# Optimization experiments

Hardware: AMD Instinct MI355X
Metric: run time of the kernel (lower is better)

The kernel has to match this reference:

```python
import jax, jax.numpy as jnp
import numpy as np

B, S, D = 2, 2048, 1024
H, DH = 16, 64
DM = 4096
NEG = 1e10


def setup_inputs() -> dict:
    key = jax.random.key(0)
    ks = jax.random.split(key, 8)
    sc = 1.0 / np.sqrt(D)
    return {
        "x": jax.random.normal(ks[0], (B, S, D), jnp.float32),
        "W_Q": jax.random.normal(ks[1], (H, DH, D), jnp.float32) * sc,
        "W_K": jax.random.normal(ks[2], (H, DH, D), jnp.float32) * sc,
        "W_V": jax.random.normal(ks[3], (H, DH, D), jnp.float32) * sc,
        "W_O": jax.random.normal(ks[4], (D, H * DH), jnp.float32) * sc,
        "W_in": jax.random.normal(ks[5], (DM, D), jnp.float32) * sc,
        "b_in": jnp.zeros((DM,), jnp.float32),
        "W_out": jax.random.normal(ks[6], (D, DM), jnp.float32) * sc,
        "b_out": jnp.zeros((D,), jnp.float32),
    }


def reference(x, W_Q, W_K, W_V, W_O, W_in, b_in, W_out, b_out):
    b, s, d = x.shape
    d_head = W_Q.shape[1]
    # --- Attention (faithful to original einsum/mask formulation) ---
    q = jnp.einsum('ihd,bpd->biph', W_Q, x)
    k = jnp.einsum('ihd,bpd->biph', W_K, x)
    v = jnp.einsum('ihd,bpd->biph', W_V, x)
    scores = jnp.einsum('biph,biqh->biqp', k, q)  # [b,i,q,p]
    # original: t.tril(scores) - 1e10 * (1 - triu(ones)) ; mask buffer is triu
    triu = jnp.triu(jnp.ones((s, s), x.dtype))
    masked = jnp.tril(scores) - NEG * (1.0 - triu)
    attn = jax.nn.softmax(masked / np.sqrt(d_head), axis=-1)
    z = jnp.einsum('biph,biqp->biqh', v, attn)          # [b,i,q,h]
    z_flat = z.transpose(0, 2, 1, 3).reshape(b, s, -1)   # b q (i h)
    attn_out = jnp.einsum('df,bqf->bqd', W_O, z_flat)
    # --- Block residual structure (as written: x = attn(x); x = x + x) ---
    mid = attn_out + attn_out
    # --- MLP ---
    pre = jnp.einsum('md,bpd->bpm', W_in, mid) + b_in
    h = jax.nn.relu(pre)
    mlp_out = jnp.einsum('dm,bpm->bpd', W_out, h) + b_out
    return mid + mlp_out
```

## Files before the change

kernel.cpp:

```cpp
#include <hip/hip_runtime.h>
#include <hip/hip_bf16.h>
#include <stdint.h>

typedef unsigned short ushort_t;
typedef __attribute__((ext_vector_type(8))) short short8;
typedef __attribute__((ext_vector_type(4))) float floatx4;

#define DEV __device__ __forceinline__

DEV ushort_t f2b(float f) {
  uint32_t x = __float_as_uint(f);
  uint32_t r = (x + 0x7FFFu + ((x >> 16) & 1u)) >> 16;
  return (ushort_t)r;
}
DEV float b2f(ushort_t u) { return __uint_as_float(((uint32_t)u) << 16); }

DEV void async16(const ushort_t* g, ushort_t* l) {
  __builtin_amdgcn_global_load_lds(
      (const __attribute__((address_space(1))) void*)g,
      (__attribute__((address_space(3))) void*)l, 16, 0, 0);
}

struct Cvt7 {
  const float* src[7];
  ushort_t* dst[7];
  float scale[7];
  unsigned start[8];
};
__global__ void cvt_all(Cvt7 a) {
  unsigned idx = blockIdx.x * blockDim.x + threadIdx.x;
  if (idx >= a.start[7]) return;
  int seg = 0;
#pragma unroll
  for (int j = 1; j < 7; j++) seg += (idx >= a.start[j]) ? 1 : 0;
  unsigned off = idx - a.start[seg];
  float sc = a.scale[seg];
  float4 v = ((const float4*)a.src[seg])[off];
  ((ushort4*)a.dst[seg])[off] =
      make_ushort4(f2b(v.x * sc), f2b(v.y * sc), f2b(v.z * sc), f2b(v.w * sc));
}

template <int MODE, int MT, int SWZ>
__launch_bounds__(256)
__global__ void gemm_bt(const ushort_t* __restrict__ A, const ushort_t* __restrict__ Bm,
                        int M, int N, int Kd, int ldk,
                        ushort_t* __restrict__ outB, float* __restrict__ outF,
                        const float* __restrict__ bias) {
  constexpr int TM = 32 * MT;
  __shared__ alignas(16) ushort_t As[TM * 64];
  __shared__ alignas(16) ushort_t Bs[128 * 64];
  const int tid = threadIdx.x;
  const int wave = tid >> 6, lane = tid & 63;
  const int wm = wave >> 1, wn = wave & 1;

  int bx, by;
  if constexpr (SWZ == 1) {
    const int f = blockIdx.x + gridDim.x * blockIdx.y;
    by = (f & 7) + 8 * (f / (8 * gridDim.x));
    bx = (f >> 3) % gridDim.x;
  } else if constexpr (SWZ == 2) {
    const int x = blockIdx.x, y = blockIdx.y;
    bx = 2 * (x & 3) + (y & 1);
    by = (y >> 1) + 32 * (x >> 2);
  } else {
    bx = blockIdx.x; by = blockIdx.y;
  }
  const int m0 = by * TM, n0 = bx * 128;
  const int kz = blockIdx.z * Kd;

  floatx4 acc[MT][4];
#pragma unroll
  for (int i = 0; i < MT; i++)
#pragma unroll
    for (int j = 0; j < 4; j++) acc[i][j] = (floatx4){0.f, 0.f, 0.f, 0.f};

  const int r8 = lane >> 3;
  const int scol = (((lane & 7) ^ (r8 & 7)) * 8);
  const ushort_t* gA = A + (size_t)(m0 + wave * (TM / 4) + r8) * ldk + kz + scol;
  const ushort_t* gB = Bm + (size_t)(n0 + wave * 32 + r8) * ldk + kz + scol;
  ushort_t* lA = As + wave * (TM / 4) * 64;
  ushort_t* lB = Bs + wave * 2048;

  const int fr = lane & 15, fq = lane >> 4;
  const int sw = fr & 7;
  const ushort_t* rdA = As + (wm * 16 * MT + fr) * 64;
  const ushort_t* rdB = Bs + (wn * 64 + fr) * 64;

  for (int k0 = 0; k0 < Kd; k0 += 64) {
#pragma unroll
    for (int j = 0; j < MT; j++) async16(gA + (size_t)j * 8 * ldk, lA + j * 512);
#pragma unroll
    for (int j = 0; j < 4; j++) async16(gB + (size_t)j * 8 * ldk, lB + j * 512);
    gA += 64; gB += 64;
    __syncthreads();
#pragma unroll
    for (int h = 0; h < 2; h++) {
      const int co = ((h * 4 + fq) ^ sw) * 8;
      short8 af[MT], bfv[4];
#pragma unroll
      for (int mt = 0; mt < MT; mt++) af[mt] = *(const short8*)(rdA + mt * 16 * 64 + co);
#pragma unroll
      for (int nt = 0; nt < 4; nt++) bfv[nt] = *(const short8*)(rdB + nt * 16 * 64 + co);
#pragma unroll
      for (int mt = 0; mt < MT; mt++)
#pragma unroll
        for (int nt = 0; nt < 4; nt++)
          acc[mt][nt] = __builtin_amdgcn_mfma_f32_16x16x32_bf16(af[mt], bfv[nt], acc[mt][nt], 0, 0, 0);
    }
    __syncthreads();
  }

  const int crow = m0 + wm * 16 * MT + (lane >> 4) * 4;
  const int ccol = n0 + wn * 64 + (lane & 15);
#pragma unroll
  for (int mt = 0; mt < MT; mt++)
#pragma unroll
    for (int nt = 0; nt < 4; nt++) {
      floatx4 a = acc[mt][nt];
#pragma unroll
      for (int r = 0; r < 4; r++) {
        const int gm = crow + mt * 16 + r;
        const int gn = ccol + nt * 16;
        const size_t idx = (size_t)gm * N + gn;
        float v = a[r];
        if constexpr (MODE == 0) {
          outB[idx] = f2b(v);
        } else if constexpr (MODE == 1) {
          outB[idx] = f2b(v);
          outF[idx] = v + bias[gn];
        } else if constexpr (MODE == 2) {
          float t = v + bias[gn];
          outB[idx] = f2b(t > 0.f ? t : 0.f);
        } else if constexpr (MODE == 5) {
          unsafeAtomicAdd(&outF[idx], v);
        }
      }
    }
}

template <int MODE>
__launch_bounds__(512, 2)
__global__ void gemm256(const ushort_t* __restrict__ A, const ushort_t* __restrict__ Bm,
                        int M, int N, int Kd, int ldk,
                        ushort_t* __restrict__ outB, float* __restrict__ outF,
                        const float* __restrict__ bias) {
  __shared__ alignas(16) ushort_t As[4][256 * 32];
  __shared__ alignas(16) ushort_t Bs[4][256 * 32];
  const int tid = threadIdx.x;
  const int lane = tid & 63;
  const int wave = tid >> 6;
  const int wm = wave >> 2, wn = wave & 3;

  const int gy = gridDim.y;
  int f = blockIdx.x + gridDim.x * blockIdx.y;
  {
    const int nwg = gridDim.x * gy;
    const int q = nwg >> 3, rr = nwg & 7;
    const int xcd = f & 7, ix = f >> 3;
    f = (xcd < rr ? xcd * (q + 1) : rr * (q + 1) + (xcd - rr) * q) + ix;
  }
  const int bx = f / gy, by = f - gy * bx;
  const int m0 = by * 256, n0 = bx * 256;
  const size_t kz = (size_t)blockIdx.z * Kd;

  floatx4 acc[8][4];
#pragma unroll
  for (int i = 0; i < 8; i++)
#pragma unroll
    for (int j = 0; j < 4; j++) acc[i][j] = (floatx4){0.f, 0.f, 0.f, 0.f};

  const int rloc = tid >> 2, cch = tid & 3;
  const int gcol = ((cch ^ ((rloc >> 1) & 3)) * 8);
  const ushort_t* gA = A + (size_t)(m0 + rloc) * ldk + kz + gcol;
  const ushort_t* gB = Bm + (size_t)(n0 + rloc) * ldk + kz + gcol;
  const int lofs = rloc * 32 + cch * 8;

#define STGA32(bufi, kofs)                                              \
  {                                                                     \
    async16(gA + (kofs), &As[bufi][lofs]);                              \
    async16(gA + (size_t)128 * ldk + (kofs), &As[bufi][4096 + lofs]);   \
  }
#define STGB32(bufi, kofs)                                              \
  {                                                                     \
    async16(gB + (kofs), &Bs[bufi][lofs]);                              \
    async16(gB + (size_t)128 * ldk + (kofs), &Bs[bufi][4096 + lofs]);   \
  }

  const int NT = Kd >> 5;
  STGA32(0, 0) STGB32(0, 0)
  if (NT > 1) { STGA32(1, 32) STGB32(1, 32) }
  if (NT > 2) { STGA32(2, 64) STGB32(2, 64) }
  if (NT > 2) asm volatile("s_waitcnt vmcnt(8)" ::: "memory");
  else if (NT > 1) asm volatile("s_waitcnt vmcnt(4)" ::: "memory");
  else asm volatile("s_waitcnt vmcnt(0)" ::: "memory");
  __builtin_amdgcn_s_barrier();

  const int fr = lane & 15, fq = lane >> 4;
  const int co = ((fq ^ ((fr >> 1) & 3)) * 8);
  const int aoff = (wm * 128 + fr) * 32 + co;
  const int boff = (wn * 64 + fr) * 32 + co;

  for (int kt = 0; kt < NT; ++kt) {
    const int cb = kt & 3;
    const int pb = (kt + 3) & 3;
    const int kof = (kt + 3) * 32;
    const bool sp = (kt + 3) < NT;
    const ushort_t* Ab = As[cb];
    const ushort_t* Bb = Bs[cb];
    short8 av[4], bv[4];

#pragma unroll
    for (int i = 0; i < 4; i++) av[i] = *(const short8*)(Ab + aoff + i * 512);
#pragma unroll
    for (int j = 0; j < 4; j++) bv[j] = *(const short8*)(Bb + boff + j * 512);
    if (sp) STGA32(pb, kof)
    __builtin_amdgcn_s_barrier();
    asm volatile("s_waitcnt lgkmcnt(0)" ::: "memory");
    __builtin_amdgcn_s_setprio(1);
#pragma unroll
    for (int i = 0; i < 4; i++)
#pragma unroll
      for (int j = 0; j < 4; j++)
        acc[i][j] = __builtin_amdgcn_mfma_f32_16x16x32_bf16(av[i], bv[j], acc[i][j], 0, 0, 0);
    __builtin_amdgcn_s_setprio(0);
    __builtin_amdgcn_s_barrier();

#pragma unroll
    for (int i = 0; i < 4; i++) av[i] = *(const short8*)(Ab + aoff + 2048 + i * 512);
    if (sp) STGB32(pb, kof)
    __builtin_amdgcn_s_barrier();
    asm volatile("s_waitcnt lgkmcnt(0)" ::: "memory");
    __builtin_amdgcn_s_setprio(1);
#pragma unroll
    for (int i = 0; i < 4; i++)
#pragma unroll
      for (int j = 0; j < 4; j++)
        acc[4 + i][j] = __builtin_amdgcn_mfma_f32_16x16x32_bf16(av[i], bv[j], acc[4 + i][j], 0, 0, 0);
    __builtin_amdgcn_s_setprio(0);
    if (kt + 3 < NT) asm volatile("s_waitcnt vmcnt(8)" ::: "memory");
    else if (kt + 2 < NT) asm volatile("s_waitcnt vmcnt(4)" ::: "memory");
    else asm volatile("s_waitcnt vmcnt(0)" ::: "memory");
    __builtin_amdgcn_s_barrier();
  }
#undef STGA32
#undef STGB32

  const int crow = m0 + wm * 128 + (lane >> 4) * 4;
  const int ccol = n0 + wn * 64 + (lane & 15);
#pragma unroll
  for (int mt = 0; mt < 8; mt++)
#pragma unroll
    for (int nt = 0; nt < 4; nt++) {
      floatx4 a = acc[mt][nt];
#pragma unroll
      for (int r = 0; r < 4; r++) {
        const int gm = crow + mt * 16 + r;
        const int gn = ccol + nt * 16;
        const size_t idx = (size_t)gm * N + gn;
        if constexpr (MODE == 0) {
          outB[idx] = f2b(a[r]);
        } else if constexpr (MODE == 2) {
          float t = a[r] + bias[gn];
          outB[idx] = f2b(t > 0.f ? t : 0.f);
        } else {
          outF[idx] = a[r];
        }
      }
    }
}

__launch_bounds__(256)
__global__ void attn1(const ushort_t* __restrict__ qkv,
                      float* __restrict__ eG, float* __restrict__ psumG) {
  const int c = blockIdx.x & 63;
  const int i = (blockIdx.x >> 6) & 15;
  const int b = blockIdx.x >> 10;
  const int t = threadIdx.x, wave = t >> 6, h = t & 63;
  const size_t rowbase = (size_t)b * 2048 * 3072;
  float vacc = 0.f;
#pragma unroll
  for (int r = 0; r < 8; r++) {
    const int s = c * 32 + wave * 8 + r;
    const size_t rb = rowbase + (size_t)s * 3072 + i * 64 + h;
    float q = b2f(qkv[rb]);
    float k = b2f(qkv[rb + 1024]);
    float v = b2f(qkv[rb + 2048]);
    float d = q * k;
#pragma unroll
    for (int off = 32; off > 0; off >>= 1) d += __shfl_xor(d, off, 64);
    if (h == 0) eG[((size_t)(b * 16 + i)) * 2048 + s] = __expf(d * 0.125f);
    vacc += v;
  }
  __shared__ float vs[4][64];
  vs[wave][h] = vacc;
  __syncthreads();
  if (t < 64)
    psumG[(((size_t)(b * 16 + i)) * 64 + c) * 64 + t] =
        vs[0][t] + vs[1][t] + vs[2][t] + vs[3][t];
}

__launch_bounds__(256)
__global__ void attn2(const ushort_t* __restrict__ qkv,
                      const float* __restrict__ eG, const float* __restrict__ psumG,
                      ushort_t* __restrict__ Z) {
  const int wave = threadIdx.x >> 6, h = threadIdx.x & 63;
  const int c = (blockIdx.x & 15) * 4 + wave;
  const int i = (blockIdx.x >> 4) & 15;
  const int b = blockIdx.x >> 8;
  const size_t rowbase = (size_t)b * 2048 * 3072;
  const size_t pbase = ((size_t)(b * 16 + i)) * 64;
  float run = 0.f;
#pragma unroll 8
  for (int cc = c + 1; cc < 64; cc++) run += psumG[(pbase + cc) * 64 + h];
  const size_t ebase = ((size_t)(b * 16 + i)) * 2048;
  for (int t4 = 1; t4 >= 0; t4--) {
    float vv[16], ee[16];
#pragma unroll
    for (int j = 0; j < 16; j++) {
      const int s = c * 32 + t4 * 16 + j;
      vv[j] = b2f(qkv[rowbase + (size_t)s * 3072 + 2048 + i * 64 + h]);
      ee[j] = eG[ebase + s];
    }
#pragma unroll
    for (int j = 15; j >= 0; j--) {
      const int s = c * 32 + t4 * 16 + j;
      float z = (ee[j] * vv[j] + run) / (ee[j] + (float)(2047 - s));
      Z[((size_t)b * 2048 + s) * 1024 + i * 64 + h] = f2b(z);
      run += vv[j];
    }
  }
}

extern "C" void kernel_launch(void* const* d_in, const int* in_sizes, int n_in,
                              void* d_out, int out_size, void* d_ws, size_t ws_size,
                              hipStream_t stream) {
  const float* x     = (const float*)d_in[0];
  const float* W_Q   = (const float*)d_in[1];
  const float* W_K   = (const float*)d_in[2];
  const float* W_V   = (const float*)d_in[3];
  const float* W_O   = (const float*)d_in[4];
  const float* W_in  = (const float*)d_in[5];
  const float* b_in  = (const float*)d_in[6];
  const float* W_out = (const float*)d_in[7];
  const float* b_out = (const float*)d_in[8];
  float* out = (float*)d_out;

  char* base = (char*)d_ws;
  const size_t MB = 1048576;
  ushort_t* Xb    = (ushort_t*)(base + 0 * MB);
  ushort_t* Wqkv  = (ushort_t*)(base + 8 * MB);
  ushort_t* WOb   = (ushort_t*)(base + 14 * MB);
  ushort_t* Z     = (ushort_t*)(base + 16 * MB);
  ushort_t* QKV   = (ushort_t*)(base + 24 * MB);
  ushort_t* midb  = (ushort_t*)(base + 48 * MB);
  ushort_t* Winb  = (ushort_t*)(base + 56 * MB);
  ushort_t* Woutb = (ushort_t*)(base + 64 * MB);
  ushort_t* Hb    = (ushort_t*)(base + 72 * MB);
  float*    psumG = (float*)(base + 72 * MB);
  float*    eG    = (float*)(base + 72 * MB + 524288);

  Cvt7 ca;
  ca.src[0] = x;     ca.dst[0] = Xb;               ca.scale[0] = 1.f;
  ca.src[1] = W_Q;   ca.dst[1] = Wqkv;             ca.scale[1] = 1.f;
  ca.src[2] = W_K;   ca.dst[2] = Wqkv + 1048576;   ca.scale[2] = 1.f;
  ca.src[3] = W_V;   ca.dst[3] = Wqkv + 2097152;   ca.scale[3] = 1.f;
  ca.src[4] = W_O;   ca.dst[4] = WOb;              ca.scale[4] = 2.f;
  ca.src[5] = W_in;  ca.dst[5] = Winb;             ca.scale[5] = 1.f;
  ca.src[6] = W_out; ca.dst[6] = Woutb;            ca.scale[6] = 1.f;
  unsigned n4s[7] = {1048576, 262144, 262144, 262144, 262144, 1048576, 1048576};
  unsigned acc4 = 0;
  for (int j = 0; j < 7; j++) { ca.start[j] = acc4; acc4 += n4s[j]; }
  ca.start[7] = acc4;
  cvt_all<<<dim3((acc4 + 255) / 256), dim3(256), 0, stream>>>(ca);

  gemm_bt<0, 4, 0><<<dim3(24, 32), 256, 0, stream>>>(Xb, Wqkv, 4096, 3072, 1024, 1024,
                                                     QKV, nullptr, nullptr);
  attn1<<<dim3(2048), 256, 0, stream>>>(QKV, eG, psumG);
  attn2<<<dim3(512), 256, 0, stream>>>(QKV, eG, psumG, Z);
  gemm_bt<1, 2, 1><<<dim3(8, 64), 256, 0, stream>>>(Z, WOb, 4096, 1024, 1024, 1024,
                                                    midb, out, b_out);
  gemm256<2><<<dim3(16, 16), 512, 0, stream>>>(midb, Winb, 4096, 4096, 1024, 1024,
                                               Hb, nullptr, b_in);
  gemm_bt<5, 2, 2><<<dim3(8, 64, 2), 256, 0, stream>>>(Hb, Woutb, 4096, 1024, 2048, 4096,
                                                       nullptr, out, nullptr);
}
```

Baseline: 286.5 us.

## Rewrite 256x256 GEMM with BK=64 double buffering and use it for QKV projection

Replaces the 4-stage BK=32 pipeline of the 256x256 GEMM with a 2-stage BK=64 double buffer using a new swizzled LDS layout. The MFMA work is split into four quadrant phases so A and B fragments are reused across phases with fewer LDS reads. The QKV projection also moves from the smaller-tile gemm_bt kernel to this 256-tile kernel, launched on a 12x16 grid. Risks: prefetch depth is only one stage and waits on vmcnt(0) every iteration, and the QKV grid of 192 blocks may underfill the GPU.

```diff
diff --git a/kernel.cpp b/kernel.cpp
--- a/kernel.cpp
+++ b/kernel.cpp
@@ -140,12 +140,12 @@
 
 template <int MODE>
 __launch_bounds__(512, 2)
-__global__ void gemm256(const ushort_t* __restrict__ A, const ushort_t* __restrict__ Bm,
-                        int M, int N, int Kd, int ldk,
-                        ushort_t* __restrict__ outB, float* __restrict__ outF,
-                        const float* __restrict__ bias) {
-  __shared__ alignas(16) ushort_t As[4][256 * 32];
-  __shared__ alignas(16) ushort_t Bs[4][256 * 32];
+__global__ void gemm256v2(const ushort_t* __restrict__ A, const ushort_t* __restrict__ Bm,
+                          int M, int N, int Kd, int ldk,
+                          ushort_t* __restrict__ outB, float* __restrict__ outF,
+                          const float* __restrict__ bias) {
+  __shared__ alignas(16) ushort_t As[2][2][8192];
+  __shared__ alignas(16) ushort_t Bs[2][2][8192];
   const int tid = threadIdx.x;
   const int lane = tid & 63;
   const int wave = tid >> 6;
@@ -169,81 +169,116 @@
 #pragma unroll
     for (int j = 0; j < 4; j++) acc[i][j] = (floatx4){0.f, 0.f, 0.f, 0.f};
 
-  const int rloc = tid >> 2, cch = tid & 3;
-  const int gcol = ((cch ^ ((rloc >> 1) & 3)) * 8);
-  const ushort_t* gA = A + (size_t)(m0 + rloc) * ldk + kz + gcol;
-  const ushort_t* gB = Bm + (size_t)(n0 + rloc) * ldk + kz + gcol;
-  const int lofs = rloc * 32 + cch * 8;
-
-#define STGA32(bufi, kofs)                                              \
-  {                                                                     \
-    async16(gA + (kofs), &As[bufi][lofs]);                              \
-    async16(gA + (size_t)128 * ldk + (kofs), &As[bufi][4096 + lofs]);   \
-  }
-#define STGB32(bufi, kofs)                                              \
-  {                                                                     \
-    async16(gB + (kofs), &Bs[bufi][lofs]);                              \
-    async16(gB + (size_t)128 * ldk + (kofs), &Bs[bufi][4096 + lofs]);   \
-  }
-
-  const int NT = Kd >> 5;
-  STGA32(0, 0) STGB32(0, 0)
-  if (NT > 1) { STGA32(1, 32) STGB32(1, 32) }
-  if (NT > 2) { STGA32(2, 64) STGB32(2, 64) }
-  if (NT > 2) asm volatile("s_waitcnt vmcnt(8)" ::: "memory");
-  else if (NT > 1) asm volatile("s_waitcnt vmcnt(4)" ::: "memory");
-  else asm volatile("s_waitcnt vmcnt(0)" ::: "memory");
+  const int srow = tid >> 3;
+  const int scol = ((tid & 7) * 8) ^ (((tid >> 3) & 1) << 5);
+  const ushort_t* gAs = A + (size_t)(m0 + srow) * ldk + kz + scol;
+  const ushort_t* gBs = Bm + (size_t)(n0 + srow) * ldk + kz + scol;
+  const int soff = tid * 8;
+
+#define STA(d, h, kof)                                                      \
+  {                                                                         \
+    async16(gAs + (size_t)((h) * 128) * ldk + (kof), &As[d][h][soff]);      \
+    async16(gAs + (size_t)((h) * 128 + 64) * ldk + (kof), &As[d][h][4096 + soff]); \
+  }
+#define STB(d, h, kof)                                                      \
+  {                                                                         \
+    async16(gBs + (size_t)((h) * 128) * ldk + (kof), &Bs[d][h][soff]);      \
+    async16(gBs + (size_t)((h) * 128 + 64) * ldk + (kof), &Bs[d][h][4096 + soff]); \
+  }
+
+  const int NT = Kd >> 6;
+  STA(0, 0, 0) STA(0, 1, 0) STB(0, 0, 0) STB(0, 1, 0)
+  asm volatile("s_waitcnt vmcnt(0)" ::: "memory");
   __builtin_amdgcn_s_barrier();
 
   const int fr = lane & 15, fq = lane >> 4;
-  const int co = ((fq ^ ((fr >> 1) & 3)) * 8);
-  const int aoff = (wm * 128 + fr) * 32 + co;
-  const int boff = (wn * 64 + fr) * 32 + co;
-
-  for (int kt = 0; kt < NT; ++kt) {
-    const int cb = kt & 3;
-    const int pb = (kt + 3) & 3;
-    const int kof = (kt + 3) * 32;
-    const bool sp = (kt + 3) < NT;
-    const ushort_t* Ab = As[cb];
-    const ushort_t* Bb = Bs[cb];
-    short8 av[4], bv[4];
-
-#pragma unroll
-    for (int i = 0; i < 4; i++) av[i] = *(const short8*)(Ab + aoff + i * 512);
-#pragma unroll
-    for (int j = 0; j < 4; j++) bv[j] = *(const short8*)(Bb + boff + j * 512);
-    if (sp) STGA32(pb, kof)
+  const int kso0 = (fr & 1) << 5;
+  const int kso1 = 32 - kso0;
+  const int abase = fr * 64 + fq * 8;
+  const int bbase = (wn & 1) * 4096 + fr * 64 + fq * 8;
+
+  for (int t = 0; t < NT; ++t) {
+    const int d = t & 1, o = d ^ 1;
+    const ushort_t* Ah = &As[d][wm][0];
+    const ushort_t* Bh = &Bs[d][wn >> 1][0];
+    const int kof = (t + 1) << 6;
+    const bool st = (t + 1) < NT;
+    short8 a0[4][2], b01[2][2], b23[2][2];
+
+#pragma unroll
+    for (int mi = 0; mi < 4; mi++) {
+      a0[mi][0] = *(const short8*)(Ah + abase + mi * 1024 + kso0);
+      a0[mi][1] = *(const short8*)(Ah + abase + mi * 1024 + kso1);
+    }
+#pragma unroll
+    for (int ni = 0; ni < 2; ni++) {
+      b01[ni][0] = *(const short8*)(Bh + bbase + ni * 1024 + kso0);
+      b01[ni][1] = *(const short8*)(Bh + bbase + ni * 1024 + kso1);
+    }
+    if (st) { STA(o, 0, kof) STA(o, 1, kof) }
     __builtin_amdgcn_s_barrier();
     asm volatile("s_waitcnt lgkmcnt(0)" ::: "memory");
     __builtin_amdgcn_s_setprio(1);
 #pragma unroll
-    for (int i = 0; i < 4; i++)
-#pragma unroll
-      for (int j = 0; j < 4; j++)
-        acc[i][j] = __builtin_amdgcn_mfma_f32_16x16x32_bf16(av[i], bv[j], acc[i][j], 0, 0, 0);
+    for (int mi = 0; mi < 4; mi++)
+#pragma unroll
+      for (int ni = 0; ni < 2; ni++) {
+        acc[mi][ni] = __builtin_amdgcn_mfma_f32_16x16x32_bf16(a0[mi][0], b01[ni][0], acc[mi][ni], 0, 0, 0);
+        acc[mi][ni] = __builtin_amdgcn_mfma_f32_16x16x32_bf16(a0[mi][1], b01[ni][1], acc[mi][ni], 0, 0, 0);
+      }
     __builtin_amdgcn_s_setprio(0);
     __builtin_amdgcn_s_barrier();
 
 #pragma unroll
-    for (int i = 0; i < 4; i++) av[i] = *(const short8*)(Ab + aoff + 2048 + i * 512);
-    if (sp) STGB32(pb, kof)
+    for (int ni = 0; ni < 2; ni++) {
+      b23[ni][0] = *(const short8*)(Bh + bbase + (ni + 2) * 1024 + kso0);
+      b23[ni][1] = *(const short8*)(Bh + bbase + (ni + 2) * 1024 + kso1);
+    }
+    if (st) { STB(o, 0, kof) STB(o, 1, kof) }
     __builtin_amdgcn_s_barrier();
     asm volatile("s_waitcnt lgkmcnt(0)" ::: "memory");
     __builtin_amdgcn_s_setprio(1);
 #pragma unroll
-    for (int i = 0; i < 4; i++)
-#pragma unroll
-      for (int j = 0; j < 4; j++)
-        acc[4 + i][j] = __builtin_amdgcn_mfma_f32_16x16x32_bf16(av[i], bv[j], acc[4 + i][j], 0, 0, 0);
+    for (int mi = 0; mi < 4; mi++)
+#pragma unroll
+      for (int ni = 0; ni < 2; ni++) {
+        acc[mi][ni + 2] = __builtin_amdgcn_mfma_f32_16x16x32_bf16(a0[mi][0], b23[ni][0], acc[mi][ni + 2], 0, 0, 0);
+        acc[mi][ni + 2] = __builtin_amdgcn_mfma_f32_16x16x32_bf16(a0[mi][1], b23[ni][1], acc[mi][ni + 2], 0, 0, 0);
+      }
     __builtin_amdgcn_s_setprio(0);
-    if (kt + 3 < NT) asm volatile("s_waitcnt vmcnt(8)" ::: "memory");
-    else if (kt + 2 < NT) asm volatile("s_waitcnt vmcnt(4)" ::: "memory");
-    else asm volatile("s_waitcnt vmcnt(0)" ::: "memory");
-    __builtin_amdgcn_s_barrier();
-  }
-#undef STGA32
-#undef STGB32
+    __builtin_amdgcn_s_barrier();
+
+#pragma unroll
+    for (int mi = 0; mi < 4; mi++) {
+      a0[mi][0] = *(const short8*)(Ah + abase + (mi + 4) * 1024 + kso0);
+      a0[mi][1] = *(const short8*)(Ah + abase + (mi + 4) * 1024 + kso1);
+    }
+    __builtin_amdgcn_s_barrier();
+    asm volatile("s_waitcnt lgkmcnt(0)" ::: "memory");
+    __builtin_amdgcn_s_setprio(1);
+#pragma unroll
+    for (int mi = 0; mi < 4; mi++)
+#pragma unroll
+      for (int ni = 0; ni < 2; ni++) {
+        acc[mi + 4][ni + 2] = __builtin_amdgcn_mfma_f32_16x16x32_bf16(a0[mi][0], b23[ni][0], acc[mi + 4][ni + 2], 0, 0, 0);
+        acc[mi + 4][ni + 2] = __builtin_amdgcn_mfma_f32_16x16x32_bf16(a0[mi][1], b23[ni][1], acc[mi + 4][ni + 2], 0, 0, 0);
+      }
+    __builtin_amdgcn_s_setprio(0);
+
+    __builtin_amdgcn_s_setprio(1);
+#pragma unroll
+    for (int mi = 0; mi < 4; mi++)
+#pragma unroll
+      for (int ni = 0; ni < 2; ni++) {
+        acc[mi + 4][ni] = __builtin_amdgcn_mfma_f32_16x16x32_bf16(a0[mi][0], b01[ni][0], acc[mi + 4][ni], 0, 0, 0);
+        acc[mi + 4][ni] = __builtin_amdgcn_mfma_f32_16x16x32_bf16(a0[mi][1], b01[ni][1], acc[mi + 4][ni], 0, 0, 0);
+      }
+    __builtin_amdgcn_s_setprio(0);
+    if (st) asm volatile("s_waitcnt vmcnt(0)" ::: "memory");
+    __builtin_amdgcn_s_barrier();
+  }
+#undef STA
+#undef STB
 
   const int crow = m0 + wm * 128 + (lane >> 4) * 4;
   const int ccol = n0 + wn * 64 + (lane & 15);
@@ -260,8 +295,8 @@
         if constexpr (MODE == 0) {
           outB[idx] = f2b(a[r]);
         } else if constexpr (MODE == 2) {
-          float t = a[r] + bias[gn];
-          outB[idx] = f2b(t > 0.f ? t : 0.f);
+          float t2 = a[r] + bias[gn];
+          outB[idx] = f2b(t2 > 0.f ? t2 : 0.f);
         } else {
           outF[idx] = a[r];
         }
@@ -373,14 +408,14 @@
   ca.start[7] = acc4;
   cvt_all<<<dim3((acc4 + 255) / 256), dim3(256), 0, stream>>>(ca);
 
-  gemm_bt<0, 4, 0><<<dim3(24, 32), 256, 0, stream>>>(Xb, Wqkv, 4096, 3072, 1024, 1024,
-                                                     QKV, nullptr, nullptr);
+  gemm256v2<0><<<dim3(12, 16), 512, 0, stream>>>(Xb, Wqkv, 4096, 3072, 1024, 1024,
+                                                 QKV, nullptr, nullptr);
   attn1<<<dim3(2048), 256, 0, stream>>>(QKV, eG, psumG);
   attn2<<<dim3(512), 256, 0, stream>>>(QKV, eG, psumG, Z);
   gemm_bt<1, 2, 1><<<dim3(8, 64), 256, 0, stream>>>(Z, WOb, 4096, 1024, 1024, 1024,
                                                     midb, out, b_out);
-  gemm256<2><<<dim3(16, 16), 512, 0, stream>>>(midb, Winb, 4096, 4096, 1024, 1024,
-                                               Hb, nullptr, b_in);
+  gemm256v2<2><<<dim3(16, 16), 512, 0, stream>>>(midb, Winb, 4096, 4096, 1024, 1024,
+                                                 Hb, nullptr, b_in);
   gemm_bt<5, 2, 2><<<dim3(8, 64, 2), 256, 0, stream>>>(Hb, Woutb, 4096, 1024, 2048, 4096,
                                                        nullptr, out, nullptr);
 }
```

Result: slower. 304.0 us (+6.1%).
